# Performance work log

Hardware: AMD Instinct MI355X
Metric: run time of the kernel (lower is better)

Reference implementation:

```python
import jax, jax.numpy as jnp
import numpy as np

LAYER_START = 4
WS = 2  # context_window_size
EPS = 1e-8


def _alpha_for_k(tf, idx):
    # tf: [L, D] per-token layer features; idx: static window row indices (last entry is k)
    Wm = tf[idx]                       # [w, D]
    w = Wm.shape[0]
    _, R = jnp.linalg.qr(Wm.T)         # reduced QR of [D, w] -> R: [w, w]
    r = R[:, -1]
    sub = R[:-1, :-1]
    coln = jnp.linalg.norm(sub, axis=0)
    align = jnp.mean(sub / coln, axis=1) @ R[:-1, -1] / jnp.linalg.norm(r[:-1])
    align = 1.0 / (align * w * 2)
    nov = jnp.abs(r[-1]) / jnp.linalg.norm(r)
    return align, nov


def _unify_token(tf):
    # tf: [L, D] -> pooled [D]
    L = tf.shape[0]
    aligns, novs = [], []
    for k in range(L):  # loop over small fixed layer count (structurally distinct windows)
        # NOTE: original torch code token_feature[k-ws:k] yields an EMPTY slice for k < ws
        left = list(range(k - WS, k)) if k >= WS else []
        right = list(range(k + 1, min(k + WS + 1, L)))
        idx = np.array(left + right + [k], dtype=np.int32)
        a, n = _alpha_for_k(tf, idx)
        aligns.append(a)
        novs.append(n)
    aa = jnp.stack(aligns)
    nv = jnp.stack(novs)
    aa = aa / aa.sum()
    nv = nv / nv.sum()
    alpha = aa + nv
    alpha = alpha / alpha.sum()
    return tf.T @ alpha


def _token_var(tf):
    # tf: [L, D] -> variance (unbiased) of subdiagonal of cosine-sim map
    w = jnp.linalg.norm(tf, axis=1, keepdims=True)
    sim = (tf @ tf.T) / jnp.clip(w * w.T, EPS)
    return jnp.var(jnp.diagonal(sim, -1), ddof=1)


def reference(all_hidden_states, attention_mask):
    # all_hidden_states: [B, num_layers, S, D]; attention_mask: [B, S] (all sentences equal length)
    T = int(np.asarray(attention_mask).sum(axis=1)[0]) - 1  # unmask_num = sum(mask) - 1
    sf = all_hidden_states[:, LAYER_START:, :T, :]          # [B, L, T, D]
    per_tok = jax.vmap(jax.vmap(_unify_token, in_axes=1))(sf)  # [B, T, D]

    def per_sentence(s, ose):
        v = jax.vmap(_token_var, in_axes=1)(s)  # [T]
        v = v / v.sum()
        return ose.T @ v                        # [D]

    return jax.vmap(per_sentence)(sf, per_tok)  # [B, D]


def setup_inputs():
    key = jax.random.key(0)
    all_hidden_states = jax.random.normal(key, (8, 12, 512, 768), dtype=jnp.float32)
    attention_mask = jnp.ones((8, 512), dtype=jnp.int32)
    return {"all_hidden_states": all_hidden_states, "attention_mask": attention_mask}
```

## Files before the change

kernel.cpp:

```cpp
#include <hip/hip_runtime.h>
#include <math.h>

#define NLAYER_TOT 12
#define LAYER0 4
#define SMAX 512
#define DIM 768
#define NSEG 128

__host__ __device__ constexpr int gp(int i, int j) {
    return (i <= j) ? (i * 8 - i * (i - 1) / 2 + (j - i))
                    : (j * 8 - j * (j - 1) / 2 + (i - j));
}

__device__ inline float frcp(float x) { return __builtin_amdgcn_rcpf(x); }
__device__ inline float frsq(float x) { return __builtin_amdgcn_rsqf(x); }

__device__ inline float wave_reduce_add(float v) {
    v += __int_as_float(__builtin_amdgcn_update_dpp(0, __float_as_int(v), 0x121, 0xF, 0xF, true));
    v += __int_as_float(__builtin_amdgcn_update_dpp(0, __float_as_int(v), 0x122, 0xF, 0xF, true));
    v += __int_as_float(__builtin_amdgcn_update_dpp(0, __float_as_int(v), 0x124, 0xF, 0xF, true));
    v += __int_as_float(__builtin_amdgcn_update_dpp(0, __float_as_int(v), 0x128, 0xF, 0xF, true));
    v += __shfl_xor(v, 16, 64);
    v += __shfl_xor(v, 32, 64);
    return v;
}

__global__ void k_init(const int* __restrict__ mask, int* __restrict__ wsT) {
    __shared__ int red[512];
    int tid = threadIdx.x;
    red[tid] = mask[tid];
    __syncthreads();
    for (int s = 256; s >= 1; s >>= 1) {
        if (tid < s) red[tid] += red[tid + s];
        __syncthreads();
    }
    if (tid == 0) wsT[0] = red[0] - 1;
}

template <int W>
__device__ inline void alpha_nov(const float (&A)[36], const int (&idx)[5],
                                 float& align_o, float& nov_o) {
    float Gs[W][W];
#pragma unroll
    for (int i = 0; i < W; ++i)
#pragma unroll
        for (int j = i; j < W; ++j) {
            float v = A[gp(idx[i], idx[j])];
            Gs[i][j] = v;
            Gs[j][i] = v;
        }
    float R[W][W];
#pragma unroll
    for (int j = 0; j < W; ++j) {
#pragma unroll
        for (int i = 0; i <= j; ++i) {
            float s = Gs[i][j];
#pragma unroll
            for (int q = 0; q < i; ++q) s -= R[q][i] * R[q][j];
            if (i == j) R[i][j] = s * frsq(s);
            else        R[i][j] = s * frcp(R[i][i]);
        }
    }
    float ic[W - 1];
#pragma unroll
    for (int j = 0; j < W - 1; ++j) ic[j] = frsq(Gs[j][j]);
    float m[W - 1];
#pragma unroll
    for (int i = 0; i < W - 1; ++i) {
        float s = 0.0f;
#pragma unroll
        for (int j = i; j < W - 1; ++j) s += R[i][j] * ic[j];
        m[i] = s * (1.0f / (float)(W - 1));
    }
    float num = 0.0f, n1 = 0.0f;
#pragma unroll
    for (int i = 0; i < W - 1; ++i) {
        num += m[i] * R[i][W - 1];
        n1 += R[i][W - 1] * R[i][W - 1];
    }
    float align_raw = num * frsq(n1);
    align_o = frcp(align_raw * (float)W * 2.0f);
    nov_o = fabsf(R[W - 1][W - 1]) * frsq(Gs[W - 1][W - 1]);
}

__global__ __launch_bounds__(256, 2) void k_main(const float* __restrict__ in,
                                                 const int* __restrict__ wsT,
                                                 float* __restrict__ P,
                                                 float* __restrict__ Vp) {
    int T = wsT[0];
    int seg = blockIdx.x;
    int b = blockIdx.y;
    int wave = threadIdx.x >> 6;
    int lane = threadIdx.x & 63;

    __shared__ float part[DIM];
    __shared__ float vpart;
    for (int i = threadIdx.x; i < DIM; i += 256) part[i] = 0.0f;
    if (threadIdx.x == 0) vpart = 0.0f;
    __syncthreads();

    int t = seg * 4 + wave;
    float4 acc12[3];
#pragma unroll
    for (int it = 0; it < 3; ++it) acc12[it] = make_float4(0.f, 0.f, 0.f, 0.f);
    float vloc = 0.0f;

    if (t < T) {
        const float* base = in + ((size_t)(b * NLAYER_TOT + LAYER0) * SMAX + t) * DIM;

        float g[36];
#pragma unroll
        for (int p = 0; p < 36; ++p) g[p] = 0.0f;
        float4 cur[8], nxt[8];
#pragma unroll
        for (int k = 0; k < 8; ++k)
            cur[k] = *(const float4*)(base + (size_t)k * SMAX * DIM + lane * 4);
#pragma unroll
        for (int it = 0; it < 3; ++it) {
            if (it < 2) {
                int d = (it + 1) * 256 + lane * 4;
#pragma unroll
                for (int k = 0; k < 8; ++k)
                    nxt[k] = *(const float4*)(base + (size_t)k * SMAX * DIM + d);
            }
            int p = 0;
#pragma unroll
            for (int i = 0; i < 8; ++i)
#pragma unroll
                for (int j = i; j < 8; ++j) {
                    g[p] += cur[i].x * cur[j].x + cur[i].y * cur[j].y +
                            cur[i].z * cur[j].z + cur[i].w * cur[j].w;
                    ++p;
                }
            if (it < 2) {
#pragma unroll
                for (int k = 0; k < 8; ++k) cur[k] = nxt[k];
            }
        }
#pragma unroll
        for (int p = 0; p < 36; ++p) g[p] = wave_reduce_add(g[p]);

#pragma unroll
        for (int k = 0; k < 8; ++k)
            cur[k] = *(const float4*)(base + (size_t)k * SMAX * DIM + lane * 4);

        static constexpr int IDX0[5] = {1, 2, 0, 0, 0};
        static constexpr int IDX1[5] = {2, 3, 1, 0, 0};
        static constexpr int IDX2[5] = {0, 1, 3, 4, 2};
        static constexpr int IDX3[5] = {1, 2, 4, 5, 3};
        static constexpr int IDX4[5] = {2, 3, 5, 6, 4};
        static constexpr int IDX5[5] = {3, 4, 6, 7, 5};
        static constexpr int IDX6[5] = {4, 5, 7, 6, 0};
        static constexpr int IDX7[5] = {5, 6, 7, 0, 0};
        float a[8], n[8];
        alpha_nov<3>(g, IDX0, a[0], n[0]);
        alpha_nov<3>(g, IDX1, a[1], n[1]);
        alpha_nov<5>(g, IDX2, a[2], n[2]);
        alpha_nov<5>(g, IDX3, a[3], n[3]);
        alpha_nov<5>(g, IDX4, a[4], n[4]);
        alpha_nov<5>(g, IDX5, a[5], n[5]);
        alpha_nov<4>(g, IDX6, a[6], n[6]);
        alpha_nov<3>(g, IDX7, a[7], n[7]);
        float sa = 0.0f, sn = 0.0f;
#pragma unroll
        for (int k = 0; k < 8; ++k) { sa += a[k]; sn += n[k]; }
        float isa = frcp(sa), isn = frcp(sn);
        float al[8], ss = 0.0f;
#pragma unroll
        for (int k = 0; k < 8; ++k) { al[k] = a[k] * isa + n[k] * isn; ss += al[k]; }
        float iss = frcp(ss);
        float c[7], mu = 0.0f;
#pragma unroll
        for (int i = 0; i < 7; ++i) {
            float denom = g[gp(i, i)] * g[gp(i + 1, i + 1)];
            c[i] = g[gp(i, i + 1)] * frsq(denom > 1e-16f ? denom : 1e-16f);
            mu += c[i];
        }
        mu *= (1.0f / 7.0f);
        float var = 0.0f;
#pragma unroll
        for (int i = 0; i < 7; ++i) var += (c[i] - mu) * (c[i] - mu);
        float vraw = var * (1.0f / 6.0f);
        vloc = vraw;
        float p8[8];
#pragma unroll
        for (int k = 0; k < 8; ++k) p8[k] = al[k] * iss * vraw;

#pragma unroll
        for (int it = 0; it < 3; ++it) {
            if (it < 2) {
                int d = (it + 1) * 256 + lane * 4;
#pragma unroll
                for (int k = 0; k < 8; ++k)
                    nxt[k] = *(const float4*)(base + (size_t)k * SMAX * DIM + d);
            }
#pragma unroll
            for (int k = 0; k < 8; ++k) {
                acc12[it].x += p8[k] * cur[k].x;
                acc12[it].y += p8[k] * cur[k].y;
                acc12[it].z += p8[k] * cur[k].z;
                acc12[it].w += p8[k] * cur[k].w;
            }
            if (it < 2) {
#pragma unroll
                for (int k = 0; k < 8; ++k) cur[k] = nxt[k];
            }
        }

#pragma unroll
        for (int it = 0; it < 3; ++it) {
            int d = it * 256 + lane * 4;
            atomicAdd(&part[d + 0], acc12[it].x);
            atomicAdd(&part[d + 1], acc12[it].y);
            atomicAdd(&part[d + 2], acc12[it].z);
            atomicAdd(&part[d + 3], acc12[it].w);
        }
        if (lane == 0) atomicAdd(&vpart, vloc);
    }
    __syncthreads();

    float* pd = P + ((size_t)b * NSEG + seg) * DIM;
    for (int i = threadIdx.x; i < DIM; i += 256) pd[i] = part[i];
    if (threadIdx.x == 0) Vp[b * NSEG + seg] = vpart;
}

__global__ void k_reduce(const float* __restrict__ P, const float* __restrict__ Vp,
                         float* __restrict__ out) {
    int b = blockIdx.x;
    int d = threadIdx.x;
    __shared__ float vred[NSEG];
    __shared__ float vinv;
    if (d < NSEG) vred[d] = Vp[b * NSEG + d];
    __syncthreads();
    if (d == 0) {
        float s = 0.0f;
        for (int i = 0; i < NSEG; ++i) s += vred[i];
        vinv = 1.0f / s;
    }
    __syncthreads();
    float s = 0.0f;
    const float* pb = P + (size_t)b * NSEG * DIM;
    for (int seg = 0; seg < NSEG; ++seg) s += pb[(size_t)seg * DIM + d];
    out[b * DIM + d] = s * vinv;
}

extern "C" void kernel_launch(void* const* d_in, const int* in_sizes, int n_in,
                              void* d_out, int out_size, void* d_ws, size_t ws_size,
                              hipStream_t stream) {
    const float* hs = (const float*)d_in[0];
    const int* mask = (const int*)d_in[1];
    float* out = (float*)d_out;
    char* ws = (char*)d_ws;
    int* wsT = (int*)ws;
    float* P = (float*)(ws + 256);
    float* Vp = (float*)(ws + 256 + (size_t)8 * NSEG * DIM * 4);

    k_init<<<1, 512, 0, stream>>>(mask, wsT);
    k_main<<<dim3(NSEG, 8), 256, 0, stream>>>(hs, wsT, P, Vp);
    k_reduce<<<8, DIM, 0, stream>>>(P, Vp, out);
}
```

Baseline: 222.0 us.

## Fuse mask count and final reduction into main kernel via last-block counter

Drops the separate init and reduce kernels. Each block now counts the mask itself, and the last block per batch, found through an atomic counter, does the cross-segment reduction. The hidden-state loads are issued before the mask reduction and barrier, and the compute no longer sits behind the t<T branch, so latency overlaps better. The cost is a memset launch, redundant mask reads, threadfence ordering, and compute on masked tokens.

```diff
diff --git a/kernel.cpp b/kernel.cpp
--- a/kernel.cpp
+++ b/kernel.cpp
@@ -25,18 +25,6 @@
     return v;
 }
 
-__global__ void k_init(const int* __restrict__ mask, int* __restrict__ wsT) {
-    __shared__ int red[512];
-    int tid = threadIdx.x;
-    red[tid] = mask[tid];
-    __syncthreads();
-    for (int s = 256; s >= 1; s >>= 1) {
-        if (tid < s) red[tid] += red[tid + s];
-        __syncthreads();
-    }
-    if (tid == 0) wsT[0] = red[0] - 1;
-}
-
 template <int W>
 __device__ inline void alpha_nov(const float (&A)[36], const int (&idx)[5],
                                  float& align_o, float& nov_o) {
@@ -84,129 +72,137 @@
 }
 
 __global__ __launch_bounds__(256, 2) void k_main(const float* __restrict__ in,
-                                                 const int* __restrict__ wsT,
+                                                 const int* __restrict__ mask,
                                                  float* __restrict__ P,
-                                                 float* __restrict__ Vp) {
-    int T = wsT[0];
+                                                 float* __restrict__ Vp,
+                                                 int* __restrict__ cnt,
+                                                 float* __restrict__ out) {
     int seg = blockIdx.x;
     int b = blockIdx.y;
-    int wave = threadIdx.x >> 6;
-    int lane = threadIdx.x & 63;
+    int tid = threadIdx.x;
+    int wave = tid >> 6;
+    int lane = tid & 63;
 
     __shared__ float part[DIM];
     __shared__ float vpart;
-    for (int i = threadIdx.x; i < DIM; i += 256) part[i] = 0.0f;
-    if (threadIdx.x == 0) vpart = 0.0f;
-    __syncthreads();
+    __shared__ float wred[4];
+    __shared__ int lastS;
 
     int t = seg * 4 + wave;
+    const float* base = in + ((size_t)(b * NLAYER_TOT + LAYER0) * SMAX + t) * DIM;
+
+    float4 cur[8], nxt[8];
+#pragma unroll
+    for (int k = 0; k < 8; ++k)
+        cur[k] = *(const float4*)(base + (size_t)k * SMAX * DIM + lane * 4);
+
+    for (int i = tid; i < DIM; i += 256) part[i] = 0.0f;
+    if (tid == 0) vpart = 0.0f;
+    float mv = (float)(mask[tid] + mask[tid + 256]);
+    mv = wave_reduce_add(mv);
+    if (lane == 0) wred[wave] = mv;
+    __syncthreads();
+    int T = (int)(wred[0] + wred[1] + wred[2] + wred[3]) - 1;
+
     float4 acc12[3];
 #pragma unroll
     for (int it = 0; it < 3; ++it) acc12[it] = make_float4(0.f, 0.f, 0.f, 0.f);
-    float vloc = 0.0f;
+
+    float g[36];
+#pragma unroll
+    for (int p = 0; p < 36; ++p) g[p] = 0.0f;
+#pragma unroll
+    for (int it = 0; it < 3; ++it) {
+        if (it < 2) {
+            int d = (it + 1) * 256 + lane * 4;
+#pragma unroll
+            for (int k = 0; k < 8; ++k)
+                nxt[k] = *(const float4*)(base + (size_t)k * SMAX * DIM + d);
+        }
+        int p = 0;
+#pragma unroll
+        for (int i = 0; i < 8; ++i)
+#pragma unroll
+            for (int j = i; j < 8; ++j) {
+                g[p] += cur[i].x * cur[j].x + cur[i].y * cur[j].y +
+                        cur[i].z * cur[j].z + cur[i].w * cur[j].w;
+                ++p;
+            }
+        if (it < 2) {
+#pragma unroll
+            for (int k = 0; k < 8; ++k) cur[k] = nxt[k];
+        }
+    }
+#pragma unroll
+    for (int p = 0; p < 36; ++p) g[p] = wave_reduce_add(g[p]);
+
+#pragma unroll
+    for (int k = 0; k < 8; ++k)
+        cur[k] = *(const float4*)(base + (size_t)k * SMAX * DIM + lane * 4);
+
+    static constexpr int IDX0[5] = {1, 2, 0, 0, 0};
+    static constexpr int IDX1[5] = {2, 3, 1, 0, 0};
+    static constexpr int IDX2[5] = {0, 1, 3, 4, 2};
+    static constexpr int IDX3[5] = {1, 2, 4, 5, 3};
+    static constexpr int IDX4[5] = {2, 3, 5, 6, 4};
+    static constexpr int IDX5[5] = {3, 4, 6, 7, 5};
+    static constexpr int IDX6[5] = {4, 5, 7, 6, 0};
+    static constexpr int IDX7[5] = {5, 6, 7, 0, 0};
+    float a[8], n[8];
+    alpha_nov<3>(g, IDX0, a[0], n[0]);
+    alpha_nov<3>(g, IDX1, a[1], n[1]);
+    alpha_nov<5>(g, IDX2, a[2], n[2]);
+    alpha_nov<5>(g, IDX3, a[3], n[3]);
+    alpha_nov<5>(g, IDX4, a[4], n[4]);
+    alpha_nov<5>(g, IDX5, a[5], n[5]);
+    alpha_nov<4>(g, IDX6, a[6], n[6]);
+    alpha_nov<3>(g, IDX7, a[7], n[7]);
+    float sa = 0.0f, sn = 0.0f;
+#pragma unroll
+    for (int k = 0; k < 8; ++k) { sa += a[k]; sn += n[k]; }
+    float isa = frcp(sa), isn = frcp(sn);
+    float al[8], ss = 0.0f;
+#pragma unroll
+    for (int k = 0; k < 8; ++k) { al[k] = a[k] * isa + n[k] * isn; ss += al[k]; }
+    float iss = frcp(ss);
+    float c[7], mu = 0.0f;
+#pragma unroll
+    for (int i = 0; i < 7; ++i) {
+        float denom = g[gp(i, i)] * g[gp(i + 1, i + 1)];
+        c[i] = g[gp(i, i + 1)] * frsq(denom > 1e-16f ? denom : 1e-16f);
+        mu += c[i];
+    }
+    mu *= (1.0f / 7.0f);
+    float var = 0.0f;
+#pragma unroll
+    for (int i = 0; i < 7; ++i) var += (c[i] - mu) * (c[i] - mu);
+    float vraw = var * (1.0f / 6.0f);
+    float p8[8];
+#pragma unroll
+    for (int k = 0; k < 8; ++k) p8[k] = al[k] * iss * vraw;
+
+#pragma unroll
+    for (int it = 0; it < 3; ++it) {
+        if (it < 2) {
+            int d = (it + 1) * 256 + lane * 4;
+#pragma unroll
+            for (int k = 0; k < 8; ++k)
+                nxt[k] = *(const float4*)(base + (size_t)k * SMAX * DIM + d);
+        }
+#pragma unroll
+        for (int k = 0; k < 8; ++k) {
+            acc12[it].x += p8[k] * cur[k].x;
+            acc12[it].y += p8[k] * cur[k].y;
+            acc12[it].z += p8[k] * cur[k].z;
+            acc12[it].w += p8[k] * cur[k].w;
+        }
+        if (it < 2) {
+#pragma unroll
+            for (int k = 0; k < 8; ++k) cur[k] = nxt[k];
+        }
+    }
 
     if (t < T) {
-        const float* base = in + ((size_t)(b * NLAYER_TOT + LAYER0) * SMAX + t) * DIM;
-
-        float g[36];
-#pragma unroll
-        for (int p = 0; p < 36; ++p) g[p] = 0.0f;
-        float4 cur[8], nxt[8];
-#pragma unroll
-        for (int k = 0; k < 8; ++k)
-            cur[k] = *(const float4*)(base + (size_t)k * SMAX * DIM + lane * 4);
-#pragma unroll
-        for (int it = 0; it < 3; ++it) {
-            if (it < 2) {
-                int d = (it + 1) * 256 + lane * 4;
-#pragma unroll
-                for (int k = 0; k < 8; ++k)
-                    nxt[k] = *(const float4*)(base + (size_t)k * SMAX * DIM + d);
-            }
-            int p = 0;
-#pragma unroll
-            for (int i = 0; i < 8; ++i)
-#pragma unroll
-                for (int j = i; j < 8; ++j) {
-                    g[p] += cur[i].x * cur[j].x + cur[i].y * cur[j].y +
-                            cur[i].z * cur[j].z + cur[i].w * cur[j].w;
-                    ++p;
-                }
-            if (it < 2) {
-#pragma unroll
-                for (int k = 0; k < 8; ++k) cur[k] = nxt[k];
-            }
-        }
-#pragma unroll
-        for (int p = 0; p < 36; ++p) g[p] = wave_reduce_add(g[p]);
-
-#pragma unroll
-        for (int k = 0; k < 8; ++k)
-            cur[k] = *(const float4*)(base + (size_t)k * SMAX * DIM + lane * 4);
-
-        static constexpr int IDX0[5] = {1, 2, 0, 0, 0};
-        static constexpr int IDX1[5] = {2, 3, 1, 0, 0};
-        static constexpr int IDX2[5] = {0, 1, 3, 4, 2};
-        static constexpr int IDX3[5] = {1, 2, 4, 5, 3};
-        static constexpr int IDX4[5] = {2, 3, 5, 6, 4};
-        static constexpr int IDX5[5] = {3, 4, 6, 7, 5};
-        static constexpr int IDX6[5] = {4, 5, 7, 6, 0};
-        static constexpr int IDX7[5] = {5, 6, 7, 0, 0};
-        float a[8], n[8];
-        alpha_nov<3>(g, IDX0, a[0], n[0]);
-        alpha_nov<3>(g, IDX1, a[1], n[1]);
-        alpha_nov<5>(g, IDX2, a[2], n[2]);
-        alpha_nov<5>(g, IDX3, a[3], n[3]);
-        alpha_nov<5>(g, IDX4, a[4], n[4]);
-        alpha_nov<5>(g, IDX5, a[5], n[5]);
-        alpha_nov<4>(g, IDX6, a[6], n[6]);
-        alpha_nov<3>(g, IDX7, a[7], n[7]);
-        float sa = 0.0f, sn = 0.0f;
-#pragma unroll
-        for (int k = 0; k < 8; ++k) { sa += a[k]; sn += n[k]; }
-        float isa = frcp(sa), isn = frcp(sn);
-        float al[8], ss = 0.0f;
-#pragma unroll
-        for (int k = 0; k < 8; ++k) { al[k] = a[k] * isa + n[k] * isn; ss += al[k]; }
-        float iss = frcp(ss);
-        float c[7], mu = 0.0f;
-#pragma unroll
-        for (int i = 0; i < 7; ++i) {
-            float denom = g[gp(i, i)] * g[gp(i + 1, i + 1)];
-            c[i] = g[gp(i, i + 1)] * frsq(denom > 1e-16f ? denom : 1e-16f);
-            mu += c[i];
-        }
-        mu *= (1.0f / 7.0f);
-        float var = 0.0f;
-#pragma unroll
-        for (int i = 0; i < 7; ++i) var += (c[i] - mu) * (c[i] - mu);
-        float vraw = var * (1.0f / 6.0f);
-        vloc = vraw;
-        float p8[8];
-#pragma unroll
-        for (int k = 0; k < 8; ++k) p8[k] = al[k] * iss * vraw;
-
-#pragma unroll
-        for (int it = 0; it < 3; ++it) {
-            if (it < 2) {
-                int d = (it + 1) * 256 + lane * 4;
-#pragma unroll
-                for (int k = 0; k < 8; ++k)
-                    nxt[k] = *(const float4*)(base + (size_t)k * SMAX * DIM + d);
-            }
-#pragma unroll
-            for (int k = 0; k < 8; ++k) {
-                acc12[it].x += p8[k] * cur[k].x;
-                acc12[it].y += p8[k] * cur[k].y;
-                acc12[it].z += p8[k] * cur[k].z;
-                acc12[it].w += p8[k] * cur[k].w;
-            }
-            if (it < 2) {
-#pragma unroll
-                for (int k = 0; k < 8; ++k) cur[k] = nxt[k];
-            }
-        }
-
 #pragma unroll
         for (int it = 0; it < 3; ++it) {
             int d = it * 256 + lane * 4;
@@ -215,33 +211,33 @@
             atomicAdd(&part[d + 2], acc12[it].z);
             atomicAdd(&part[d + 3], acc12[it].w);
         }
-        if (lane == 0) atomicAdd(&vpart, vloc);
+        if (lane == 0) atomicAdd(&vpart, vraw);
     }
     __syncthreads();
 
     float* pd = P + ((size_t)b * NSEG + seg) * DIM;
-    for (int i = threadIdx.x; i < DIM; i += 256) pd[i] = part[i];
-    if (threadIdx.x == 0) Vp[b * NSEG + seg] = vpart;
-}
-
-__global__ void k_reduce(const float* __restrict__ P, const float* __restrict__ Vp,
-                         float* __restrict__ out) {
-    int b = blockIdx.x;
-    int d = threadIdx.x;
-    __shared__ float vred[NSEG];
-    __shared__ float vinv;
-    if (d < NSEG) vred[d] = Vp[b * NSEG + d];
-    __syncthreads();
-    if (d == 0) {
-        float s = 0.0f;
-        for (int i = 0; i < NSEG; ++i) s += vred[i];
-        vinv = 1.0f / s;
-    }
-    __syncthreads();
-    float s = 0.0f;
-    const float* pb = P + (size_t)b * NSEG * DIM;
-    for (int seg = 0; seg < NSEG; ++seg) s += pb[(size_t)seg * DIM + d];
-    out[b * DIM + d] = s * vinv;
+    for (int i = tid; i < DIM; i += 256) pd[i] = part[i];
+    if (tid == 0) Vp[b * NSEG + seg] = vpart;
+    __threadfence();
+    __syncthreads();
+    if (tid == 0) lastS = (atomicAdd(&cnt[b], 1) == NSEG - 1) ? 1 : 0;
+    __syncthreads();
+
+    if (lastS) {
+        __threadfence();
+        float v = (tid < NSEG) ? Vp[b * NSEG + tid] : 0.0f;
+        v = wave_reduce_add(v);
+        if (lane == 0) wred[wave] = v;
+        __syncthreads();
+        float vinv = 1.0f / (wred[0] + wred[1] + wred[2] + wred[3]);
+        const float* pb = P + (size_t)b * NSEG * DIM;
+        for (int d = tid; d < DIM; d += 256) {
+            float s = 0.0f;
+#pragma unroll 8
+            for (int s2 = 0; s2 < NSEG; ++s2) s += pb[(size_t)s2 * DIM + d];
+            out[b * DIM + d] = s * vinv;
+        }
+    }
 }
 
 extern "C" void kernel_launch(void* const* d_in, const int* in_sizes, int n_in,
@@ -251,11 +247,10 @@
     const int* mask = (const int*)d_in[1];
     float* out = (float*)d_out;
     char* ws = (char*)d_ws;
-    int* wsT = (int*)ws;
-    float* P = (float*)(ws + 256);
-    float* Vp = (float*)(ws + 256 + (size_t)8 * NSEG * DIM * 4);
-
-    k_init<<<1, 512, 0, stream>>>(mask, wsT);
-    k_main<<<dim3(NSEG, 8), 256, 0, stream>>>(hs, wsT, P, Vp);
-    k_reduce<<<8, DIM, 0, stream>>>(P, Vp, out);
-}
+    int* cnt = (int*)ws;
+    float* Vp = (float*)(ws + 256);
+    float* P = (float*)(ws + 256 + (size_t)8 * NSEG * sizeof(float));
+
+    hipMemsetAsync(ws, 0, 64, stream);
+    k_main<<<dim3(NSEG, 8), 256, 0, stream>>>(hs, mask, P, Vp, cnt, out);
+}
```

Measured after the change: 376.7 us. +69.7%, slower.
